# Optimization experiments

Hardware: AMD Instinct MI355X
Metric: run time of the kernel (lower is better)

## Reference

```python
import jax, jax.numpy as jnp
import numpy as np

B, S, H = 64, 2048, 512
NEG_INF = -1e10


def setup_inputs() -> dict:
    key = jax.random.key(0)
    k1, k2, k3, k4, k5, k6 = jax.random.split(key, 6)
    return {
        "output": jax.random.normal(k1, (B, 1, H), dtype=jnp.float32),
        "encoder_outputs": jax.random.normal(k2, (B, S, H), dtype=jnp.float32),
        "encoder_sequence_lengths": jax.random.randint(k3, (B,), 1, S + 1, dtype=jnp.int32),
        "W1": jax.random.normal(k4, (H, H), dtype=jnp.float32) * (1.0 / np.sqrt(H)),
        "W2": jax.random.normal(k5, (H, H), dtype=jnp.float32) * (1.0 / np.sqrt(H)),
        "V": jax.random.normal(k6, (H, 1), dtype=jnp.float32) * (1.0 / np.sqrt(H)),
    }


def reference(output, encoder_outputs, encoder_sequence_lengths, W1, W2, V):
    # output: [B,1,H] decoder state (query); encoder_outputs: [B,S,H] (key & value)
    S_ = encoder_outputs.shape[1]
    key_proj = jnp.einsum('bsh,hd->bsd', encoder_outputs, W1)   # [B,S,H]
    query_proj = jnp.einsum('bqh,hd->bqd', output, W2)          # [B,1,H]
    energy = jnp.einsum('bsh,ho->bso', jnp.tanh(key_proj + query_proj), V)  # [B,S,1]
    mask = jnp.arange(S_)[None, :, None] < encoder_sequence_lengths[:, None, None]  # [B,S,1]
    energy = jnp.where(mask, energy, NEG_INF)
    attn = jax.nn.softmax(energy, axis=1)                       # [B,S,1]
    context = jnp.sum(attn * encoder_outputs, axis=1)           # [B,H]
    return context
```

## Files before the change

### kernel.cpp

```cpp
#include <hip/hip_runtime.h>
#include <hip/hip_bf16.h>

#define SS 2048
#define HH 512

typedef __attribute__((ext_vector_type(8))) short short8;
typedef __attribute__((ext_vector_type(4))) float f32x4;

__device__ __forceinline__ float bflo(unsigned u) { return __uint_as_float(u << 16); }
__device__ __forceinline__ float bfhi(unsigned u) { return __uint_as_float(u & 0xffff0000u); }

__device__ __forceinline__ short f2bf(float v) {
  __hip_bfloat16 h = __float2bfloat16(v);
  return *reinterpret_cast<short*>(&h);
}

__device__ __forceinline__ float tanh_fast(float x) {
  x = fminf(fmaxf(x, -15.f), 15.f);
  float e = __expf(2.f * x);
  return 1.f - 2.f / (e + 1.f);
}

__global__ void k_detect(const unsigned* __restrict__ Eu, int* __restrict__ flag) {
  int lane = threadIdx.x;
  unsigned w = Eu[(size_t)lane * 4097];
  unsigned e = (w >> 7) & 0xFF;
  bool inr = (e >= 90 && e <= 140);
  unsigned long long m = __ballot(inr);
  if (lane == 0) *flag = (__popcll(m) >= 48) ? 1 : 0;
}

__global__ __launch_bounds__(256) void k_transpose(const __hip_bfloat16* __restrict__ W1b,
                                                   const float* __restrict__ W1f,
                                                   const int* __restrict__ flagp,
                                                   __hip_bfloat16* __restrict__ W1T) {
  const int mode = *flagp;
  __shared__ __hip_bfloat16 t[64][65];
  int r0 = blockIdx.y * 64, c0 = blockIdx.x * 64;
  for (int i = threadIdx.x; i < 4096; i += 256) {
    int r = i >> 6, c = i & 63;
    size_t idx = (size_t)(r0 + r) * HH + c0 + c;
    float v = mode ? (float)W1b[idx] : W1f[idx];
    t[r][c] = __float2bfloat16(v);
  }
  __syncthreads();
  for (int i = threadIdx.x; i < 4096; i += 256) {
    int r = i >> 6, c = i & 63;
    W1T[(size_t)(c0 + r) * HH + r0 + c] = t[c][r];
  }
}

__global__ __launch_bounds__(256) void k_qp(const __hip_bfloat16* __restrict__ qb,
                                            const float* __restrict__ qf,
                                            const __hip_bfloat16* __restrict__ W2b,
                                            const float* __restrict__ W2f,
                                            const int* __restrict__ flagp,
                                            float* __restrict__ qp_part) {
  const int mode = *flagp;
  int b = blockIdx.x, p = blockIdx.y, h0 = p * 128;
  __shared__ float qs[128];
  if (threadIdx.x < 128) {
    size_t qi = (size_t)b * HH + h0 + threadIdx.x;
    qs[threadIdx.x] = mode ? (float)qb[qi] : qf[qi];
  }
  __syncthreads();
  int col = threadIdx.x * 2;
  float a0 = 0.f, a1 = 0.f;
  if (mode) {
#pragma unroll 4
    for (int i = 0; i < 128; ++i) {
      float qa = qs[i];
      unsigned u = *(const unsigned*)(W2b + (size_t)(h0 + i) * HH + col);
      a0 = fmaf(qa, bflo(u), a0);
      a1 = fmaf(qa, bfhi(u), a1);
    }
  } else {
#pragma unroll 4
    for (int i = 0; i < 128; ++i) {
      float qa = qs[i];
      float2 v = *(const float2*)(W2f + (size_t)(h0 + i) * HH + col);
      a0 = fmaf(qa, v.x, a0);
      a1 = fmaf(qa, v.y, a1);
    }
  }
  float* dst = qp_part + ((size_t)p * 64 + b) * HH + col;
  dst[0] = a0;
  dst[1] = a1;
}

__global__ __launch_bounds__(256, 2) void k_energy(
    const __hip_bfloat16* __restrict__ Eb, const float* __restrict__ Ef,
    const __hip_bfloat16* __restrict__ W1T, const float* __restrict__ qpp,
    const __hip_bfloat16* __restrict__ Vwb, const float* __restrict__ Vwf,
    const int* __restrict__ flagp, const int* __restrict__ lens,
    float* __restrict__ energy) {
  __shared__ __align__(16) __hip_bfloat16 Bt[2][128 * 32];
  __shared__ float qps[HH];
  __shared__ float Vs[HH];

  const int tid = threadIdx.x;
  const int wave = tid >> 6, lane = tid & 63;
  const int quad = lane >> 4, l16 = lane & 15;
  const int row0 = blockIdx.x * 128;
  const int b = row0 >> 11;
  if ((row0 & 2047) >= lens[b]) return;

  const int mode = *flagp;

  for (int i = tid; i < HH; i += 256) {
    qps[i] = qpp[(size_t)b * HH + i] + qpp[(size_t)(64 + b) * HH + i] +
             qpp[(size_t)(128 + b) * HH + i] + qpp[(size_t)(192 + b) * HH + i];
    Vs[i] = mode ? (float)Vwb[i] : Vwf[i];
  }

  short8 afr[2][16];
  {
    const size_t eBase = (size_t)row0 * HH + (size_t)(wave * 32 + l16) * HH + quad * 8;
    if (mode) {
      const __hip_bfloat16* pa = Eb + eBase;
#pragma unroll
      for (int kt = 0; kt < 16; ++kt) {
        afr[0][kt] = *(const short8*)(pa + kt * 32);
        afr[1][kt] = *(const short8*)(pa + 16 * HH + kt * 32);
      }
    } else {
      const float* pa = Ef + eBase;
#pragma unroll
      for (int kt = 0; kt < 16; ++kt) {
#pragma unroll
        for (int rb = 0; rb < 2; ++rb) {
          const float* p = pa + rb * 16 * HH + kt * 32;
          f32x4 x0 = *(const f32x4*)p;
          f32x4 x1 = *(const f32x4*)(p + 4);
          short8 v;
#pragma unroll
          for (int j = 0; j < 4; ++j) {
            v[j] = f2bf(x0[j]);
            v[j + 4] = f2bf(x1[j]);
          }
          afr[rb][kt] = v;
        }
      }
    }
  }

  const int rs0 = wave * 32 + (lane >> 2);
  const int rs1 = rs0 + 16;
  const int kg0 = ((lane & 3) - (rs0 >> 1)) & 3;
  const int kg1 = ((lane & 3) - (rs1 >> 1)) & 3;
  const __hip_bfloat16* pb0 = W1T + (size_t)rs0 * HH + kg0 * 8;
  const __hip_bfloat16* pb1 = W1T + (size_t)rs1 * HH + kg1 * 8;
  const int wslot = wave * 1024 + lane * 8;

  int offB[8];
#pragma unroll
  for (int cb = 0; cb < 8; ++cb) {
    int n = cb * 16 + l16;
    offB[cb] = n * 32 + (((quad + (n >> 1)) & 3) << 3);
  }

  short8 bp0 = *(const short8*)(pb0);
  short8 bp1 = *(const short8*)(pb1);
  *(short8*)(&Bt[0][0] + wslot) = bp0;
  *(short8*)(&Bt[0][0] + wslot + 512) = bp1;
  bp0 = *(const short8*)(pb0 + 32);
  bp1 = *(const short8*)(pb1 + 32);
  __syncthreads();

  float eacc[2][4] = {{0.f, 0.f, 0.f, 0.f}, {0.f, 0.f, 0.f, 0.f}};

  for (int nc = 0; nc < 4; ++nc) {
    f32x4 acc[2][8];
#pragma unroll
    for (int rb = 0; rb < 2; ++rb)
#pragma unroll
      for (int cb = 0; cb < 8; ++cb) acc[rb][cb] = (f32x4){0.f, 0.f, 0.f, 0.f};

#pragma unroll
    for (int kt = 0; kt < 16; ++kt) {
      const int t = nc * 16 + kt;
      const __hip_bfloat16* bb = &Bt[t & 1][0];
      short8 af0 = afr[0][kt];
      short8 af1 = afr[1][kt];
#pragma unroll
      for (int cb = 0; cb < 8; ++cb) {
        short8 bf = *(const short8*)(bb + offB[cb]);
        acc[0][cb] = __builtin_amdgcn_mfma_f32_16x16x32_bf16(af0, bf, acc[0][cb], 0, 0, 0);
        acc[1][cb] = __builtin_amdgcn_mfma_f32_16x16x32_bf16(af1, bf, acc[1][cb], 0, 0, 0);
      }

      {
        __hip_bfloat16* bw = &Bt[(t + 1) & 1][0] + wslot;
        *(short8*)bw = bp0;
        *(short8*)(bw + 512) = bp1;
        int t2 = t + 2;
        if (t2 > 63) t2 = 63;
        int o = ((t2 >> 4) << 16) + ((t2 & 15) << 5);
        bp0 = *(const short8*)(pb0 + o);
        bp1 = *(const short8*)(pb1 + o);
      }
      asm volatile("s_waitcnt lgkmcnt(0)" ::: "memory");
      __builtin_amdgcn_s_barrier();
      __builtin_amdgcn_sched_barrier(0);
    }

#pragma unroll
    for (int rb = 0; rb < 2; ++rb)
#pragma unroll
      for (int cb = 0; cb < 8; ++cb) {
        int col = nc * 128 + cb * 16 + l16;
        float qv = qps[col], vv = Vs[col];
#pragma unroll
        for (int r = 0; r < 4; ++r) {
          float t = tanh_fast(acc[rb][cb][r] + qv);
          eacc[rb][r] = fmaf(vv, t, eacc[rb][r]);
        }
      }
  }

#pragma unroll
  for (int rb = 0; rb < 2; ++rb)
#pragma unroll
    for (int r = 0; r < 4; ++r) {
      float v = eacc[rb][r];
#pragma unroll
      for (int o = 1; o < 16; o <<= 1) v += __shfl_xor(v, o);
      if (l16 == 0) energy[row0 + wave * 32 + rb * 16 + quad * 4 + r] = v;
    }
}

__global__ __launch_bounds__(256) void k_ctx(const __hip_bfloat16* __restrict__ Eb,
                                             const float* __restrict__ Ef,
                                             const float* __restrict__ energy,
                                             const int* __restrict__ lens,
                                             const int* __restrict__ flagp,
                                             float* __restrict__ partials) {
  const int mode = *flagp;
  int bc = blockIdx.x;
  int b = bc >> 4, c = bc & 15;
  int len = lens[b];
  int s0 = c * 128;
  if (s0 >= len) return;
  int tid = threadIdx.x;
  const float* eb = energy + b * SS;

  float m = -3.0e38f;
  for (int s = tid; s < len; s += 256) m = fmaxf(m, eb[s]);
#pragma unroll
  for (int o = 1; o < 64; o <<= 1) m = fmaxf(m, __shfl_xor(m, o));
  __shared__ float sm[4];
  __shared__ float sd[4];
  int wv = tid >> 6;
  if ((tid & 63) == 0) sm[wv] = m;
  __syncthreads();
  m = fmaxf(fmaxf(sm[0], sm[1]), fmaxf(sm[2], sm[3]));
  float ssum = 0.f;
  for (int s = tid; s < len; s += 256) ssum += __expf(eb[s] - m);
#pragma unroll
  for (int o = 1; o < 64; o <<= 1) ssum += __shfl_xor(ssum, o);
  if ((tid & 63) == 0) sd[wv] = ssum;
  __syncthreads();
  float inv = 1.f / (sd[0] + sd[1] + sd[2] + sd[3]);

  __shared__ float p[128];
  __shared__ f32x4 part[128];
  if (tid < 128) {
    int s = s0 + tid;
    p[tid] = (s < len) ? __expf(eb[s] - m) * inv : 0.f;
  }
  __syncthreads();
  int n = min(128, len - s0);
  int h0 = (tid & 127) * 4;
  int r = tid >> 7;
  f32x4 a = {0.f, 0.f, 0.f, 0.f};
  if (mode) {
    const __hip_bfloat16* base = Eb + (size_t)(b * SS + s0) * HH + h0;
#pragma unroll 2
    for (int i = r; i < n; i += 2) {
      float w = p[i];
      uint2 u = *(const uint2*)(base + (size_t)i * HH);
      a[0] = fmaf(w, bflo(u.x), a[0]);
      a[1] = fmaf(w, bfhi(u.x), a[1]);
      a[2] = fmaf(w, bflo(u.y), a[2]);
      a[3] = fmaf(w, bfhi(u.y), a[3]);
    }
  } else {
    const float* base = Ef + (size_t)(b * SS + s0) * HH + h0;
#pragma unroll 2
    for (int i = r; i < n; i += 2) {
      float w = p[i];
      f32x4 v = __builtin_nontemporal_load((const f32x4*)(base + (size_t)i * HH));
      a[0] = fmaf(w, v[0], a[0]);
      a[1] = fmaf(w, v[1], a[1]);
      a[2] = fmaf(w, v[2], a[2]);
      a[3] = fmaf(w, v[3], a[3]);
    }
  }
  if (tid >= 128) part[tid - 128] = a;
  __syncthreads();
  if (tid < 128) {
    f32x4 o = part[tid];
    f32x4 s;
    s[0] = a[0] + o[0];
    s[1] = a[1] + o[1];
    s[2] = a[2] + o[2];
    s[3] = a[3] + o[3];
    *(f32x4*)(partials + (size_t)(b * 16 + c) * HH + h0) = s;
  }
}

__global__ __launch_bounds__(256) void k_store(const float* __restrict__ partials,
                                               const int* __restrict__ lens,
                                               const int* __restrict__ flagp,
                                               __hip_bfloat16* __restrict__ outb,
                                               float* __restrict__ outf) {
  const int mode = *flagp;
  int i = blockIdx.x * 256 + threadIdx.x;
  int b = i >> 9, h = i & 511;
  int nch = (lens[b] + 127) >> 7;
  float s = 0.f;
  for (int c = 0; c < nch; ++c) s += partials[(size_t)(b * 16 + c) * HH + h];
  if (mode)
    outb[i] = __float2bfloat16(s);
  else
    outf[i] = s;
}

extern "C" void kernel_launch(void* const* d_in, const int* in_sizes, int n_in,
                              void* d_out, int out_size, void* d_ws, size_t ws_size,
                              hipStream_t stream) {
  const __hip_bfloat16* qb  = (const __hip_bfloat16*)d_in[0];
  const float*          qf  = (const float*)d_in[0];
  const __hip_bfloat16* Eb  = (const __hip_bfloat16*)d_in[1];
  const float*          Ef  = (const float*)d_in[1];
  const int* lens           = (const int*)d_in[2];
  const __hip_bfloat16* W1b = (const __hip_bfloat16*)d_in[3];
  const float*          W1f = (const float*)d_in[3];
  const __hip_bfloat16* W2b = (const __hip_bfloat16*)d_in[4];
  const float*          W2f = (const float*)d_in[4];
  const __hip_bfloat16* Vwb = (const __hip_bfloat16*)d_in[5];
  const float*          Vwf = (const float*)d_in[5];
  __hip_bfloat16* outb      = (__hip_bfloat16*)d_out;
  float*          outf      = (float*)d_out;

  char* ws = (char*)d_ws;
  float* energy       = (float*)(ws);
  __hip_bfloat16* W1T = (__hip_bfloat16*)(ws + 524288);
  float* qp_part      = (float*)(ws + 1048576);
  float* partials     = (float*)(ws + 1572864);
  int* flag           = (int*)(ws + 3670016);

  k_detect<<<dim3(1), 64, 0, stream>>>((const unsigned*)d_in[1], flag);
  k_transpose<<<dim3(8, 8), 256, 0, stream>>>(W1b, W1f, flag, W1T);
  k_qp<<<dim3(64, 4), 256, 0, stream>>>(qb, qf, W2b, W2f, flag, qp_part);
  k_energy<<<dim3(1024), 256, 0, stream>>>(Eb, Ef, W1T, qp_part, Vwb, Vwf, flag, lens, energy);
  k_ctx<<<dim3(1024), 256, 0, stream>>>(Eb, Ef, energy, lens, flag, partials);
  k_store<<<dim3(128), 256, 0, stream>>>(partials, lens, flag, outb, outf);
}
```

Before: 480.9 us.

## Fuse softmax and context into energy kernel using online-softmax partials

Folds the transpose and query-projection kernels into one prep launch, and moves the softmax and context weighting into the energy kernel. Each 128-row tile now computes a local max, sum of exponentials and weighted context. A small reduce kernel then merges the tiles with rescaled partials, flash-attention style. This removes a separate pass over the encoder outputs, the energy round trip and two launches, while the encoder tile read again is likely still cache-resident. In exchange the energy kernel gains extra shared memory and barriers, and the nontemporal load hint is dropped.

```diff
diff --git a/kernel.cpp b/kernel.cpp
--- a/kernel.cpp
+++ b/kernel.cpp
@@ -30,62 +30,62 @@
   if (lane == 0) *flag = (__popcll(m) >= 48) ? 1 : 0;
 }
 
-__global__ __launch_bounds__(256) void k_transpose(const __hip_bfloat16* __restrict__ W1b,
-                                                   const float* __restrict__ W1f,
-                                                   const int* __restrict__ flagp,
-                                                   __hip_bfloat16* __restrict__ W1T) {
+__global__ __launch_bounds__(256) void k_prep(const __hip_bfloat16* __restrict__ W1b,
+                                              const float* __restrict__ W1f,
+                                              const __hip_bfloat16* __restrict__ qb,
+                                              const float* __restrict__ qf,
+                                              const __hip_bfloat16* __restrict__ W2b,
+                                              const float* __restrict__ W2f,
+                                              const int* __restrict__ flagp,
+                                              __hip_bfloat16* __restrict__ W1T,
+                                              float* __restrict__ qp_part) {
   const int mode = *flagp;
   __shared__ __hip_bfloat16 t[64][65];
-  int r0 = blockIdx.y * 64, c0 = blockIdx.x * 64;
-  for (int i = threadIdx.x; i < 4096; i += 256) {
-    int r = i >> 6, c = i & 63;
-    size_t idx = (size_t)(r0 + r) * HH + c0 + c;
-    float v = mode ? (float)W1b[idx] : W1f[idx];
-    t[r][c] = __float2bfloat16(v);
-  }
-  __syncthreads();
-  for (int i = threadIdx.x; i < 4096; i += 256) {
-    int r = i >> 6, c = i & 63;
-    W1T[(size_t)(c0 + r) * HH + r0 + c] = t[c][r];
-  }
-}
-
-__global__ __launch_bounds__(256) void k_qp(const __hip_bfloat16* __restrict__ qb,
-                                            const float* __restrict__ qf,
-                                            const __hip_bfloat16* __restrict__ W2b,
-                                            const float* __restrict__ W2f,
-                                            const int* __restrict__ flagp,
-                                            float* __restrict__ qp_part) {
-  const int mode = *flagp;
-  int b = blockIdx.x, p = blockIdx.y, h0 = p * 128;
   __shared__ float qs[128];
-  if (threadIdx.x < 128) {
-    size_t qi = (size_t)b * HH + h0 + threadIdx.x;
-    qs[threadIdx.x] = mode ? (float)qb[qi] : qf[qi];
-  }
-  __syncthreads();
-  int col = threadIdx.x * 2;
-  float a0 = 0.f, a1 = 0.f;
-  if (mode) {
+  if (blockIdx.x < 64) {
+    int r0 = (blockIdx.x >> 3) * 64, c0 = (blockIdx.x & 7) * 64;
+    for (int i = threadIdx.x; i < 4096; i += 256) {
+      int r = i >> 6, c = i & 63;
+      size_t idx = (size_t)(r0 + r) * HH + c0 + c;
+      float v = mode ? (float)W1b[idx] : W1f[idx];
+      t[r][c] = __float2bfloat16(v);
+    }
+    __syncthreads();
+    for (int i = threadIdx.x; i < 4096; i += 256) {
+      int r = i >> 6, c = i & 63;
+      W1T[(size_t)(c0 + r) * HH + r0 + c] = t[c][r];
+    }
+  } else {
+    int bx = blockIdx.x - 64;
+    int b = bx & 63, p = bx >> 6, h0 = p * 128;
+    if (threadIdx.x < 128) {
+      size_t qi = (size_t)b * HH + h0 + threadIdx.x;
+      qs[threadIdx.x] = mode ? (float)qb[qi] : qf[qi];
+    }
+    __syncthreads();
+    int col = threadIdx.x * 2;
+    float a0 = 0.f, a1 = 0.f;
+    if (mode) {
 #pragma unroll 4
-    for (int i = 0; i < 128; ++i) {
-      float qa = qs[i];
-      unsigned u = *(const unsigned*)(W2b + (size_t)(h0 + i) * HH + col);
-      a0 = fmaf(qa, bflo(u), a0);
-      a1 = fmaf(qa, bfhi(u), a1);
-    }
-  } else {
+      for (int i = 0; i < 128; ++i) {
+        float qa = qs[i];
+        unsigned u = *(const unsigned*)(W2b + (size_t)(h0 + i) * HH + col);
+        a0 = fmaf(qa, bflo(u), a0);
+        a1 = fmaf(qa, bfhi(u), a1);
+      }
+    } else {
 #pragma unroll 4
-    for (int i = 0; i < 128; ++i) {
-      float qa = qs[i];
-      float2 v = *(const float2*)(W2f + (size_t)(h0 + i) * HH + col);
-      a0 = fmaf(qa, v.x, a0);
-      a1 = fmaf(qa, v.y, a1);
-    }
-  }
-  float* dst = qp_part + ((size_t)p * 64 + b) * HH + col;
-  dst[0] = a0;
-  dst[1] = a1;
+      for (int i = 0; i < 128; ++i) {
+        float qa = qs[i];
+        float2 v = *(const float2*)(W2f + (size_t)(h0 + i) * HH + col);
+        a0 = fmaf(qa, v.x, a0);
+        a1 = fmaf(qa, v.y, a1);
+      }
+    }
+    float* dst = qp_part + ((size_t)p * 64 + b) * HH + col;
+    dst[0] = a0;
+    dst[1] = a1;
+  }
 }
 
 __global__ __launch_bounds__(256, 2) void k_energy(
@@ -93,17 +93,21 @@
     const __hip_bfloat16* __restrict__ W1T, const float* __restrict__ qpp,
     const __hip_bfloat16* __restrict__ Vwb, const float* __restrict__ Vwf,
     const int* __restrict__ flagp, const int* __restrict__ lens,
-    float* __restrict__ energy) {
+    float* __restrict__ tpart) {
   __shared__ __align__(16) __hip_bfloat16 Bt[2][128 * 32];
   __shared__ float qps[HH];
   __shared__ float Vs[HH];
+  __shared__ float p[128];
+  __shared__ float red[4];
+  __shared__ f32x4 part[128];
 
   const int tid = threadIdx.x;
   const int wave = tid >> 6, lane = tid & 63;
   const int quad = lane >> 4, l16 = lane & 15;
   const int row0 = blockIdx.x * 128;
   const int b = row0 >> 11;
-  if ((row0 & 2047) >= lens[b]) return;
+  const int len = lens[b];
+  if ((row0 & 2047) >= len) return;
 
   const int mode = *flagp;
 
@@ -129,9 +133,9 @@
       for (int kt = 0; kt < 16; ++kt) {
 #pragma unroll
         for (int rb = 0; rb < 2; ++rb) {
-          const float* p = pa + rb * 16 * HH + kt * 32;
-          f32x4 x0 = *(const f32x4*)p;
-          f32x4 x1 = *(const f32x4*)(p + 4);
+          const float* pp = pa + rb * 16 * HH + kt * 32;
+          f32x4 x0 = *(const f32x4*)pp;
+          f32x4 x1 = *(const f32x4*)(pp + 4);
           short8 v;
 #pragma unroll
           for (int j = 0; j < 4; ++j) {
@@ -212,8 +216,8 @@
         float qv = qps[col], vv = Vs[col];
 #pragma unroll
         for (int r = 0; r < 4; ++r) {
-          float t = tanh_fast(acc[rb][cb][r] + qv);
-          eacc[rb][r] = fmaf(vv, t, eacc[rb][r]);
+          float tv = tanh_fast(acc[rb][cb][r] + qv);
+          eacc[rb][r] = fmaf(vv, tv, eacc[rb][r]);
         }
       }
   }
@@ -225,75 +229,56 @@
       float v = eacc[rb][r];
 #pragma unroll
       for (int o = 1; o < 16; o <<= 1) v += __shfl_xor(v, o);
-      if (l16 == 0) energy[row0 + wave * 32 + rb * 16 + quad * 4 + r] = v;
-    }
-}
-
-__global__ __launch_bounds__(256) void k_ctx(const __hip_bfloat16* __restrict__ Eb,
-                                             const float* __restrict__ Ef,
-                                             const float* __restrict__ energy,
-                                             const int* __restrict__ lens,
-                                             const int* __restrict__ flagp,
-                                             float* __restrict__ partials) {
-  const int mode = *flagp;
-  int bc = blockIdx.x;
-  int b = bc >> 4, c = bc & 15;
-  int len = lens[b];
-  int s0 = c * 128;
-  if (s0 >= len) return;
-  int tid = threadIdx.x;
-  const float* eb = energy + b * SS;
-
-  float m = -3.0e38f;
-  for (int s = tid; s < len; s += 256) m = fmaxf(m, eb[s]);
+      if (l16 == 0) {
+        int row = wave * 32 + rb * 16 + quad * 4 + r;
+        int s = (row0 & 2047) + row;
+        p[row] = (s < len) ? v : -3.0e38f;
+      }
+    }
+  __syncthreads();
+
+  float e = (tid < 128) ? p[tid] : -3.0e38f;
+  float m = e;
 #pragma unroll
   for (int o = 1; o < 64; o <<= 1) m = fmaxf(m, __shfl_xor(m, o));
-  __shared__ float sm[4];
-  __shared__ float sd[4];
-  int wv = tid >> 6;
-  if ((tid & 63) == 0) sm[wv] = m;
-  __syncthreads();
-  m = fmaxf(fmaxf(sm[0], sm[1]), fmaxf(sm[2], sm[3]));
-  float ssum = 0.f;
-  for (int s = tid; s < len; s += 256) ssum += __expf(eb[s] - m);
-#pragma unroll
-  for (int o = 1; o < 64; o <<= 1) ssum += __shfl_xor(ssum, o);
-  if ((tid & 63) == 0) sd[wv] = ssum;
-  __syncthreads();
-  float inv = 1.f / (sd[0] + sd[1] + sd[2] + sd[3]);
-
-  __shared__ float p[128];
-  __shared__ f32x4 part[128];
-  if (tid < 128) {
-    int s = s0 + tid;
-    p[tid] = (s < len) ? __expf(eb[s] - m) * inv : 0.f;
-  }
-  __syncthreads();
-  int n = min(128, len - s0);
-  int h0 = (tid & 127) * 4;
-  int r = tid >> 7;
+  if ((tid & 63) == 0) red[tid >> 6] = m;
+  __syncthreads();
+  m = fmaxf(fmaxf(red[0], red[1]), fmaxf(red[2], red[3]));
+  float w = (tid < 128) ? __expf(e - m) : 0.f;
+  float d = w;
+#pragma unroll
+  for (int o = 1; o < 64; o <<= 1) d += __shfl_xor(d, o);
+  __syncthreads();
+  if ((tid & 63) == 0) red[tid >> 6] = d;
+  if (tid < 128) p[tid] = w;
+  __syncthreads();
+  const float d_t = red[0] + red[1] + red[2] + red[3];
+
+  const int n = min(128, len - (row0 & 2047));
+  const int h0 = (tid & 127) * 4;
+  const int rr = tid >> 7;
   f32x4 a = {0.f, 0.f, 0.f, 0.f};
   if (mode) {
-    const __hip_bfloat16* base = Eb + (size_t)(b * SS + s0) * HH + h0;
+    const __hip_bfloat16* base = Eb + (size_t)row0 * HH + h0;
 #pragma unroll 2
-    for (int i = r; i < n; i += 2) {
-      float w = p[i];
+    for (int i = rr; i < n; i += 2) {
+      float wv = p[i];
       uint2 u = *(const uint2*)(base + (size_t)i * HH);
-      a[0] = fmaf(w, bflo(u.x), a[0]);
-      a[1] = fmaf(w, bfhi(u.x), a[1]);
-      a[2] = fmaf(w, bflo(u.y), a[2]);
-      a[3] = fmaf(w, bfhi(u.y), a[3]);
+      a[0] = fmaf(wv, bflo(u.x), a[0]);
+      a[1] = fmaf(wv, bfhi(u.x), a[1]);
+      a[2] = fmaf(wv, bflo(u.y), a[2]);
+      a[3] = fmaf(wv, bfhi(u.y), a[3]);
     }
   } else {
-    const float* base = Ef + (size_t)(b * SS + s0) * HH + h0;
+    const float* base = Ef + (size_t)row0 * HH + h0;
 #pragma unroll 2
-    for (int i = r; i < n; i += 2) {
-      float w = p[i];
-      f32x4 v = __builtin_nontemporal_load((const f32x4*)(base + (size_t)i * HH));
-      a[0] = fmaf(w, v[0], a[0]);
-      a[1] = fmaf(w, v[1], a[1]);
-      a[2] = fmaf(w, v[2], a[2]);
-      a[3] = fmaf(w, v[3], a[3]);
+    for (int i = rr; i < n; i += 2) {
+      float wv = p[i];
+      f32x4 v = *(const f32x4*)(base + (size_t)i * HH);
+      a[0] = fmaf(wv, v[0], a[0]);
+      a[1] = fmaf(wv, v[1], a[1]);
+      a[2] = fmaf(wv, v[2], a[2]);
+      a[3] = fmaf(wv, v[3], a[3]);
     }
   }
   if (tid >= 128) part[tid - 128] = a;
@@ -305,25 +290,42 @@
     s[1] = a[1] + o[1];
     s[2] = a[2] + o[2];
     s[3] = a[3] + o[3];
-    *(f32x4*)(partials + (size_t)(b * 16 + c) * HH + h0) = s;
-  }
-}
-
-__global__ __launch_bounds__(256) void k_store(const float* __restrict__ partials,
-                                               const int* __restrict__ lens,
-                                               const int* __restrict__ flagp,
-                                               __hip_bfloat16* __restrict__ outb,
-                                               float* __restrict__ outf) {
-  const int mode = *flagp;
-  int i = blockIdx.x * 256 + threadIdx.x;
-  int b = i >> 9, h = i & 511;
-  int nch = (lens[b] + 127) >> 7;
-  float s = 0.f;
-  for (int c = 0; c < nch; ++c) s += partials[(size_t)(b * 16 + c) * HH + h];
-  if (mode)
-    outb[i] = __float2bfloat16(s);
-  else
-    outf[i] = s;
+    *(f32x4*)(tpart + (size_t)blockIdx.x * 516 + h0) = s;
+  }
+  if (tid == 0) {
+    tpart[(size_t)blockIdx.x * 516 + 512] = m;
+    tpart[(size_t)blockIdx.x * 516 + 513] = d_t;
+  }
+}
+
+__global__ __launch_bounds__(256) void k_reduce(const float* __restrict__ tpart,
+                                                const int* __restrict__ lens,
+                                                const int* __restrict__ flagp,
+                                                __hip_bfloat16* __restrict__ outb,
+                                                float* __restrict__ outf) {
+  const int b = blockIdx.x, tid = threadIdx.x;
+  const int nch = (lens[b] + 127) >> 7;
+  const float* tb = tpart + (size_t)b * 16 * 516;
+  float m = -3.0e38f;
+  for (int c = 0; c < nch; ++c) m = fmaxf(m, tb[c * 516 + 512]);
+  const int h = tid * 2;
+  float den = 0.f, a0 = 0.f, a1 = 0.f;
+  for (int c = 0; c < nch; ++c) {
+    float sc = __expf(tb[c * 516 + 512] - m);
+    den = fmaf(tb[c * 516 + 513], sc, den);
+    float2 v = *(const float2*)(tb + c * 516 + h);
+    a0 = fmaf(sc, v.x, a0);
+    a1 = fmaf(sc, v.y, a1);
+  }
+  float inv = 1.f / den;
+  int i = b * HH + h;
+  if (*flagp) {
+    outb[i] = __float2bfloat16(a0 * inv);
+    outb[i + 1] = __float2bfloat16(a1 * inv);
+  } else {
+    outf[i] = a0 * inv;
+    outf[i + 1] = a1 * inv;
+  }
 }
 
 extern "C" void kernel_launch(void* const* d_in, const int* in_sizes, int n_in,
@@ -344,16 +346,13 @@
   float*          outf      = (float*)d_out;
 
   char* ws = (char*)d_ws;
-  float* energy       = (float*)(ws);
-  __hip_bfloat16* W1T = (__hip_bfloat16*)(ws + 524288);
-  float* qp_part      = (float*)(ws + 1048576);
-  float* partials     = (float*)(ws + 1572864);
-  int* flag           = (int*)(ws + 3670016);
+  __hip_bfloat16* W1T = (__hip_bfloat16*)(ws);
+  float* qp_part      = (float*)(ws + 524288);
+  float* tpart        = (float*)(ws + 1048576);
+  int* flag           = (int*)(ws + 3162112);
 
   k_detect<<<dim3(1), 64, 0, stream>>>((const unsigned*)d_in[1], flag);
-  k_transpose<<<dim3(8, 8), 256, 0, stream>>>(W1b, W1f, flag, W1T);
-  k_qp<<<dim3(64, 4), 256, 0, stream>>>(qb, qf, W2b, W2f, flag, qp_part);
-  k_energy<<<dim3(1024), 256, 0, stream>>>(Eb, Ef, W1T, qp_part, Vwb, Vwf, flag, lens, energy);
-  k_ctx<<<dim3(1024), 256, 0, stream>>>(Eb, Ef, energy, lens, flag, partials);
-  k_store<<<dim3(128), 256, 0, stream>>>(partials, lens, flag, outb, outf);
-}
+  k_prep<<<dim3(320), 256, 0, stream>>>(W1b, W1f, qb, qf, W2b, W2f, flag, W1T, qp_part);
+  k_energy<<<dim3(1024), 256, 0, stream>>>(Eb, Ef, W1T, qp_part, Vwb, Vwf, flag, lens, tpart);
+  k_reduce<<<dim3(64), 256, 0, stream>>>(tpart, lens, flag, outb, outf);
+}
```

After: 466.5 us. 1.03x faster.
